# Kernel tuning notes

Measured on AMD Instinct MI355X. Metric: run time of the kernel, lower is better.

Reference implementation:

```python
import jax, jax.numpy as jnp
import numpy as np

B, T, I, H, F = 128, 256, 1024, 1024, 64


def setup_inputs() -> dict:
    key = jax.random.key(0)
    ks = jax.random.split(key, 12)
    s_ih = 1.0 / np.sqrt(I)
    s_hh = 1.0 / np.sqrt(H)
    s_fp = 1.0 / np.sqrt(F)
    def mk(k, shape, s):
        return jax.random.uniform(k, shape, jnp.float32, -s, s)
    inp = {
        "seq_input": jax.random.normal(ks[0], (B, T, I), jnp.float32),
        "field_pos": jax.random.normal(ks[1], (B, T, F), jnp.float32),
        # forward-direction cell params
        "W_ih_f": mk(ks[2], (4 * H, I), s_ih),
        "W_hh_f": mk(ks[3], (4 * H, H), s_hh),
        "b_f": mk(ks[4], (4 * H,), s_hh),
        "W_fp_f": mk(ks[5], (2 * H, F), s_fp),
        "b_fp_f": mk(ks[6], (2 * H,), s_fp),
        # backward-direction cell params
        "W_ih_b": mk(ks[7], (4 * H, I), s_ih),
        "W_hh_b": mk(ks[8], (4 * H, H), s_hh),
        "b_b": mk(ks[9], (4 * H,), s_hh),
        "W_fp_b": mk(ks[10], (2 * H, F), s_fp),
        "b_fp_b": mk(ks[11], (2 * H,), s_fp),
    }
    return inp


def _run_direction(xs, fps, W_ih, W_hh, b, W_fp, b_fp, rev):
    # xs: [T, B, I], fps: [T, B, F]  (time-major for scan)
    batch = xs.shape[1]
    h0 = jnp.zeros((batch, H), xs.dtype)
    c0 = jnp.zeros((batch, H), xs.dtype)

    def step(carry, inp):
        h, c = carry
        x, fp = inp
        gates = x @ W_ih.T + h @ W_hh.T + b            # [B, 4H]
        i_g, f_g, g_g, o_g = jnp.split(gates, 4, axis=-1)
        i_g = jax.nn.sigmoid(i_g)
        f_g = jax.nn.sigmoid(f_g)
        g_g = jnp.tanh(g_g)
        o_g = jax.nn.sigmoid(o_g)
        fg = fp @ W_fp.T + b_fp                        # [B, 2H] field gate
        l_g = jax.nn.sigmoid(fg[:, :H])
        d_g = jnp.tanh(fg[:, H:])
        c = f_g * c + i_g * g_g + l_g * d_g
        h = o_g * jnp.tanh(c)
        return (h, c), h

    (h_n, c_n), outs = jax.lax.scan(step, (h0, c0), (xs, fps), reverse=rev)
    # outs: [T, B, H] in original time order (scan with reverse=True already
    # restores forward ordering of stacked outputs, matching reverse(outputs))
    return outs, h_n, c_n


def reference(seq_input, field_pos,
              W_ih_f, W_hh_f, b_f, W_fp_f, b_fp_f,
              W_ih_b, W_hh_b, b_b, W_fp_b, b_fp_b):
    xs = jnp.swapaxes(seq_input, 0, 1)   # [T, B, I]
    fps = jnp.swapaxes(field_pos, 0, 1)  # [T, B, F]
    out_f, hf, cf = _run_direction(xs, fps, W_ih_f, W_hh_f, b_f, W_fp_f, b_fp_f, False)
    out_b, hb, cb = _run_direction(xs, fps, W_ih_b, W_hh_b, b_b, W_fp_b, b_fp_b, True)
    outputs = jnp.concatenate([out_f, out_b], axis=-1)   # [T, B, 2H] (torch.stack is seq-major)
    h_n = jnp.stack([hf, hb], axis=0)                    # [2, B, H]
    c_n = jnp.stack([cf, cb], axis=0)
    return outputs, h_n, c_n
```

## Files before the change

### kernel.cpp

```cpp
#include <hip/hip_runtime.h>
#include <hip/hip_bf16.h>


#define Bn 128
#define Tn 256
#define In 1024
#define Hn 1024
#define Fn 64

typedef __attribute__((ext_vector_type(8))) short short8;
typedef __attribute__((ext_vector_type(4))) short short4v;
typedef __attribute__((ext_vector_type(4))) float f32x4;

__device__ __forceinline__ unsigned short f2bf(float f) {
  __hip_bfloat16 h = __float2bfloat16(f);
  return *reinterpret_cast<unsigned short*>(&h);
}
__device__ __forceinline__ float sigm(float x) { return 1.0f / (1.0f + __expf(-x)); }
__device__ __forceinline__ float tanh_(float x) { return 1.0f - 2.0f / (1.0f + __expf(2.0f * x)); }

__global__ void f32_to_bf16_vec(const float* __restrict__ src, short* __restrict__ dst, int n4) {
  for (int i = blockIdx.x * blockDim.x + threadIdx.x; i < n4; i += gridDim.x * blockDim.x) {
    const float4 v = ((const float4*)src)[i];
    short4v o;
    o[0] = (short)f2bf(v.x); o[1] = (short)f2bf(v.y);
    o[2] = (short)f2bf(v.z); o[3] = (short)f2bf(v.w);
    ((short4v*)dst)[i] = o;
  }
}

__global__ void init_state(float* __restrict__ c_state, unsigned int* __restrict__ h0w) {
  const int i = blockIdx.x * blockDim.x + threadIdx.x;
  if (i < 2 * Bn * Hn) c_state[i] = 0.0f;
  if (i < (2 * Bn * Hn) / 2) h0w[i] = 0u;
}

__global__ __launch_bounds__(256) void lstm_step(
    const short* __restrict__ seq, const short* __restrict__ fpos,
    const short* __restrict__ Wih_f, const short* __restrict__ Whh_f,
    const short* __restrict__ Wfp_f,
    const short* __restrict__ Wih_b, const short* __restrict__ Whh_b,
    const short* __restrict__ Wfp_b,
    const float* __restrict__ b_f,  const float* __restrict__ bfp_f,
    const float* __restrict__ b_b,  const float* __restrict__ bfp_b,
    float* __restrict__ c_state,
    const short* __restrict__ h_read, short* __restrict__ h_write,
    float* __restrict__ out, int s)
{
  const int utile = blockIdx.x;
  const int mtile = blockIdx.y;
  const int dir   = blockIdx.z;
  const int t = dir ? (Tn - 1 - s) : s;
  const int j0 = utile * 16, m0 = mtile * 64;
  const int tid = threadIdx.x;
  const int lane = tid & 63, w = tid >> 6;
  const int l15 = lane & 15, lk = lane >> 4;

  const short* Wih = dir ? Wih_b : Wih_f;
  const short* Whh = dir ? Whh_b : Whh_f;
  const short* Wfp = dir ? Wfp_b : Wfp_f;
  const float* bg  = dir ? b_b   : b_f;
  const float* bfp = dir ? bfp_b : bfp_f;

  const int abat = m0 + 16 * w + l15;
  const short* xrow = seq    + ((size_t)abat * Tn + t) * In + lk * 8;
  const short* hrow = h_read + ((size_t)dir * Bn + abat) * Hn + lk * 8;

  f32x4 acc[4];
#pragma unroll
  for (int nf = 0; nf < 4; ++nf) acc[nf] = (f32x4){0.f, 0.f, 0.f, 0.f};

  const short* wr_ih[4];
  const short* wr_hh[4];
#pragma unroll
  for (int nf = 0; nf < 4; ++nf) {
    const int row = nf * Hn + j0 + l15;
    wr_ih[nf] = Wih + (size_t)row * In + lk * 8;
    wr_hh[nf] = Whh + (size_t)row * Hn + lk * 8;
  }

  for (int k = 0; k < In; k += 32) {
    const short8 a = *(const short8*)(xrow + k);
#pragma unroll
    for (int nf = 0; nf < 4; ++nf) {
      const short8 b = *(const short8*)(wr_ih[nf] + k);
      acc[nf] = __builtin_amdgcn_mfma_f32_16x16x32_bf16(a, b, acc[nf], 0, 0, 0);
    }
  }
  for (int k = 0; k < Hn; k += 32) {
    const short8 a = *(const short8*)(hrow + k);
#pragma unroll
    for (int nf = 0; nf < 4; ++nf) {
      const short8 b = *(const short8*)(wr_hh[nf] + k);
      acc[nf] = __builtin_amdgcn_mfma_f32_16x16x32_bf16(a, b, acc[nf], 0, 0, 0);
    }
  }

  f32x4 accf[2];
#pragma unroll
  for (int nf = 0; nf < 2; ++nf) accf[nf] = (f32x4){0.f, 0.f, 0.f, 0.f};
  const short* frow = fpos + ((size_t)abat * Tn + t) * Fn + lk * 8;
#pragma unroll
  for (int k = 0; k < Fn; k += 32) {
    const short8 a = *(const short8*)(frow + k);
#pragma unroll
    for (int nf = 0; nf < 2; ++nf) {
      const short8 b = *(const short8*)(Wfp + (size_t)(nf * Hn + j0 + l15) * Fn + lk * 8 + k);
      accf[nf] = __builtin_amdgcn_mfma_f32_16x16x32_bf16(a, b, accf[nf], 0, 0, 0);
    }
  }

  __shared__ float lds[4][64][17];
  __shared__ float ldsf[2][64][17];
#pragma unroll
  for (int nf = 0; nf < 4; ++nf)
#pragma unroll
    for (int r = 0; r < 4; ++r)
      lds[nf][16 * w + lk * 4 + r][l15] = acc[nf][r];
#pragma unroll
  for (int nf = 0; nf < 2; ++nf)
#pragma unroll
    for (int r = 0; r < 4; ++r)
      ldsf[nf][16 * w + lk * 4 + r][l15] = accf[nf][r];
  __syncthreads();

  const size_t OUTN = (size_t)Tn * Bn * 2 * Hn;
#pragma unroll
  for (int q = 0; q < 4; ++q) {
    const int p = tid + 256 * q;
    const int ml = p >> 4, jl = p & 15;
    const int bat = m0 + ml, j = j0 + jl;
    const float i_g = sigm (lds[0][ml][jl] + bg[j]);
    const float f_g = sigm (lds[1][ml][jl] + bg[Hn + j]);
    const float g_g = tanh_(lds[2][ml][jl] + bg[2 * Hn + j]);
    const float o_g = sigm (lds[3][ml][jl] + bg[3 * Hn + j]);
    const float l_g = sigm (ldsf[0][ml][jl] + bfp[j]);
    const float d_g = tanh_(ldsf[1][ml][jl] + bfp[Hn + j]);
    const size_t cidx = ((size_t)dir * Bn + bat) * Hn + j;
    const float c_new = f_g * c_state[cidx] + i_g * g_g + l_g * d_g;
    const float h_new = o_g * tanh_(c_new);
    c_state[cidx] = c_new;
    h_write[cidx] = (short)f2bf(h_new);
    out[((size_t)t * Bn + bat) * (2 * Hn) + (size_t)dir * Hn + j] = h_new;
    if (s == Tn - 1) {
      out[OUTN + cidx] = h_new;
      out[OUTN + (size_t)2 * Bn * Hn + cidx] = c_new;
    }
  }
}

static inline void conv(const void* src, short* dst, size_t n, hipStream_t stream) {
  int n4 = (int)(n / 4);
  int blocks = (n4 + 255) / 256; if (blocks > 8192) blocks = 8192;
  hipLaunchKernelGGL(f32_to_bf16_vec, dim3(blocks), dim3(256), 0, stream,
                     (const float*)src, dst, n4);
}

extern "C" void kernel_launch(void* const* d_in, const int* in_sizes, int n_in,
                              void* d_out, int out_size, void* d_ws, size_t ws_size,
                              hipStream_t stream) {
  (void)in_sizes; (void)n_in; (void)out_size; (void)ws_size;
  const float* b_f   = (const float*)d_in[4];
  const float* bfp_f = (const float*)d_in[6];
  const float* b_b   = (const float*)d_in[9];
  const float* bfp_b = (const float*)d_in[11];

  char* p = (char*)d_ws;
  float* c_state = (float*)p;            p += (size_t)2 * Bn * Hn * 4;
  short* h0      = (short*)p;            p += (size_t)2 * Bn * Hn * 2;
  short* h1      = (short*)p;            p += (size_t)2 * Bn * Hn * 2;
  short* seq_bf  = (short*)p;            p += (size_t)Bn * Tn * In * 2;
  short* fpos_bf = (short*)p;            p += (size_t)Bn * Tn * Fn * 2;
  short* Wih_bf[2], *Whh_bf[2], *Wfp_bf[2];
  for (int d = 0; d < 2; ++d) { Wih_bf[d] = (short*)p; p += (size_t)4 * Hn * In * 2; }
  for (int d = 0; d < 2; ++d) { Whh_bf[d] = (short*)p; p += (size_t)4 * Hn * Hn * 2; }
  for (int d = 0; d < 2; ++d) { Wfp_bf[d] = (short*)p; p += (size_t)2 * Hn * Fn * 2; }
  float* out = (float*)d_out;

  conv(d_in[0], seq_bf,   (size_t)Bn * Tn * In, stream);
  conv(d_in[1], fpos_bf,  (size_t)Bn * Tn * Fn, stream);
  conv(d_in[2], Wih_bf[0], (size_t)4 * Hn * In, stream);
  conv(d_in[3], Whh_bf[0], (size_t)4 * Hn * Hn, stream);
  conv(d_in[5], Wfp_bf[0], (size_t)2 * Hn * Fn, stream);
  conv(d_in[7], Wih_bf[1], (size_t)4 * Hn * In, stream);
  conv(d_in[8], Whh_bf[1], (size_t)4 * Hn * Hn, stream);
  conv(d_in[10], Wfp_bf[1], (size_t)2 * Hn * Fn, stream);

  hipLaunchKernelGGL(init_state, dim3((2 * Bn * Hn + 255) / 256), dim3(256), 0, stream,
                     c_state, (unsigned int*)h0);

  for (int s = 0; s < Tn; ++s) {
    const short* hr = (s & 1) ? h1 : h0;
    short* hw       = (s & 1) ? h0 : h1;
    hipLaunchKernelGGL(lstm_step, dim3(64, 2, 2), dim3(256), 0, stream,
                       seq_bf, fpos_bf,
                       Wih_bf[0], Whh_bf[0], Wfp_bf[0],
                       Wih_bf[1], Whh_bf[1], Wfp_bf[1],
                       b_f, bfp_f, b_b, bfp_b,
                       c_state, hr, hw, out, s);
  }
}
```

Baseline: 10.60 ms.

## Hoist input and field-gate projections out of the recurrence into chunked batched GEMMs

The input-to-hidden and field-position projections no longer run inside each per-timestep kernel. They are now computed for chunks of 32 timesteps by large batched GEMM kernels that write bf16 gate pre-activations, bias included. The per-step kernel then only does the recurrent h@W_hh^T product, with 512 threads per block, and adds the precomputed gates. This removes the serial dependence of the x-projection and lets it run at full GEMM parallelism, at the cost of extra workspace and bf16 rounding of the precomputed gates.

```diff
diff --git a/kernel.cpp b/kernel.cpp
--- a/kernel.cpp
+++ b/kernel.cpp
@@ -7,11 +7,17 @@
 #define In 1024
 #define Hn 1024
 #define Fn 64
+#define CH 32
 
 typedef __attribute__((ext_vector_type(8))) short short8;
 typedef __attribute__((ext_vector_type(4))) short short4v;
 typedef __attribute__((ext_vector_type(4))) float f32x4;
 
+__device__ __forceinline__ float bf2f(short u) {
+  union { unsigned int i; float f; } x;
+  x.i = ((unsigned int)(unsigned short)u) << 16;
+  return x.f;
+}
 __device__ __forceinline__ unsigned short f2bf(float f) {
   __hip_bfloat16 h = __float2bfloat16(f);
   return *reinterpret_cast<unsigned short*>(&h);
@@ -35,107 +41,159 @@
   if (i < (2 * Bn * Hn) / 2) h0w[i] = 0u;
 }
 
-__global__ __launch_bounds__(256) void lstm_step(
-    const short* __restrict__ seq, const short* __restrict__ fpos,
-    const short* __restrict__ Wih_f, const short* __restrict__ Whh_f,
-    const short* __restrict__ Wfp_f,
-    const short* __restrict__ Wih_b, const short* __restrict__ Whh_b,
-    const short* __restrict__ Wfp_b,
-    const float* __restrict__ b_f,  const float* __restrict__ bfp_f,
-    const float* __restrict__ b_b,  const float* __restrict__ bfp_b,
+__global__ __launch_bounds__(512) void precompute_gx(
+    const short* __restrict__ seq_bf,
+    const short* __restrict__ Wih_f, const short* __restrict__ Wih_b,
+    const float* __restrict__ b_f, const float* __restrict__ b_b,
+    short* __restrict__ gx, int c0)
+{
+  const int n0 = blockIdx.x * 64;
+  const int row0 = blockIdx.y * 64;
+  const int dir = blockIdx.z;
+  const int tid = threadIdx.x, lane = tid & 63, w = tid >> 6;
+  const int l15 = lane & 15, lk = lane >> 4;
+  const int mf = w & 3, nfp = w >> 2;
+
+  const short* Wih = dir ? Wih_b : Wih_f;
+  const float* bg  = dir ? b_b   : b_f;
+
+  const int grow = row0 + mf * 16 + l15;
+  const int sl = grow >> 7, bat = grow & 127;
+  const int t = dir ? (Tn - 1 - (c0 + sl)) : (c0 + sl);
+  const short* xrow = seq_bf + ((size_t)bat * Tn + t) * In + lk * 8;
+
+  const short* br[2];
+#pragma unroll
+  for (int q = 0; q < 2; ++q)
+    br[q] = Wih + (size_t)(n0 + (nfp * 2 + q) * 16 + l15) * In + lk * 8;
+
+  f32x4 acc[2];
+  acc[0] = (f32x4){0.f,0.f,0.f,0.f}; acc[1] = (f32x4){0.f,0.f,0.f,0.f};
+  for (int k = 0; k < In; k += 32) {
+    const short8 a = *(const short8*)(xrow + k);
+#pragma unroll
+    for (int q = 0; q < 2; ++q) {
+      const short8 b = *(const short8*)(br[q] + k);
+      acc[q] = __builtin_amdgcn_mfma_f32_16x16x32_bf16(a, b, acc[q], 0, 0, 0);
+    }
+  }
+#pragma unroll
+  for (int q = 0; q < 2; ++q) {
+    const int col = n0 + (nfp * 2 + q) * 16 + l15;
+    const float bias = bg[col];
+#pragma unroll
+    for (int r = 0; r < 4; ++r) {
+      const int grow2 = row0 + mf * 16 + lk * 4 + r;
+      const int sl2 = grow2 >> 7, bat2 = grow2 & 127;
+      gx[(((size_t)dir * CH + sl2) * Bn + bat2) * (4 * Hn) + col] =
+          (short)f2bf(acc[q][r] + bias);
+    }
+  }
+}
+
+__global__ __launch_bounds__(512) void precompute_fg(
+    const short* __restrict__ fpos_bf,
+    const short* __restrict__ Wfp_f, const short* __restrict__ Wfp_b,
+    const float* __restrict__ bfp_f, const float* __restrict__ bfp_b,
+    short* __restrict__ fg, int c0)
+{
+  const int n0 = blockIdx.x * 64;
+  const int row0 = blockIdx.y * 64;
+  const int dir = blockIdx.z;
+  const int tid = threadIdx.x, lane = tid & 63, w = tid >> 6;
+  const int l15 = lane & 15, lk = lane >> 4;
+  const int mf = w & 3, nfp = w >> 2;
+
+  const short* Wfp = dir ? Wfp_b : Wfp_f;
+  const float* bfp = dir ? bfp_b : bfp_f;
+
+  const int grow = row0 + mf * 16 + l15;
+  const int sl = grow >> 7, bat = grow & 127;
+  const int t = dir ? (Tn - 1 - (c0 + sl)) : (c0 + sl);
+  const short* frow = fpos_bf + ((size_t)bat * Tn + t) * Fn + lk * 8;
+
+  f32x4 acc[2];
+  acc[0] = (f32x4){0.f,0.f,0.f,0.f}; acc[1] = (f32x4){0.f,0.f,0.f,0.f};
+#pragma unroll
+  for (int k = 0; k < Fn; k += 32) {
+    const short8 a = *(const short8*)(frow + k);
+#pragma unroll
+    for (int q = 0; q < 2; ++q) {
+      const short8 b = *(const short8*)(Wfp + (size_t)(n0 + (nfp * 2 + q) * 16 + l15) * Fn + lk * 8 + k);
+      acc[q] = __builtin_amdgcn_mfma_f32_16x16x32_bf16(a, b, acc[q], 0, 0, 0);
+    }
+  }
+#pragma unroll
+  for (int q = 0; q < 2; ++q) {
+    const int col = n0 + (nfp * 2 + q) * 16 + l15;
+    const float bias = bfp[col];
+#pragma unroll
+    for (int r = 0; r < 4; ++r) {
+      const int grow2 = row0 + mf * 16 + lk * 4 + r;
+      const int sl2 = grow2 >> 7, bat2 = grow2 & 127;
+      fg[(((size_t)dir * CH + sl2) * Bn + bat2) * (2 * Hn) + col] =
+          (short)f2bf(acc[q][r] + bias);
+    }
+  }
+}
+
+__global__ __launch_bounds__(512) void lstm_step2(
+    const short* __restrict__ Whh_f, const short* __restrict__ Whh_b,
+    const short* __restrict__ gx, const short* __restrict__ fg,
     float* __restrict__ c_state,
     const short* __restrict__ h_read, short* __restrict__ h_write,
-    float* __restrict__ out, int s)
+    float* __restrict__ out, int s, int sl)
 {
-  const int utile = blockIdx.x;
-  const int mtile = blockIdx.y;
-  const int dir   = blockIdx.z;
+  const int j0 = blockIdx.x * 16;
+  const int dir = blockIdx.y;
+  const int m0 = blockIdx.z * 64;
   const int t = dir ? (Tn - 1 - s) : s;
-  const int j0 = utile * 16, m0 = mtile * 64;
-  const int tid = threadIdx.x;
-  const int lane = tid & 63, w = tid >> 6;
+  const int tid = threadIdx.x, lane = tid & 63, w = tid >> 6;
   const int l15 = lane & 15, lk = lane >> 4;
-
-  const short* Wih = dir ? Wih_b : Wih_f;
+  const int mf = w & 3, nfp = w >> 2;
+
   const short* Whh = dir ? Whh_b : Whh_f;
-  const short* Wfp = dir ? Wfp_b : Wfp_f;
-  const float* bg  = dir ? b_b   : b_f;
-  const float* bfp = dir ? bfp_b : bfp_f;
-
-  const int abat = m0 + 16 * w + l15;
-  const short* xrow = seq    + ((size_t)abat * Tn + t) * In + lk * 8;
+
+  const int abat = m0 + mf * 16 + l15;
   const short* hrow = h_read + ((size_t)dir * Bn + abat) * Hn + lk * 8;
-
-  f32x4 acc[4];
-#pragma unroll
-  for (int nf = 0; nf < 4; ++nf) acc[nf] = (f32x4){0.f, 0.f, 0.f, 0.f};
-
-  const short* wr_ih[4];
-  const short* wr_hh[4];
-#pragma unroll
-  for (int nf = 0; nf < 4; ++nf) {
-    const int row = nf * Hn + j0 + l15;
-    wr_ih[nf] = Wih + (size_t)row * In + lk * 8;
-    wr_hh[nf] = Whh + (size_t)row * Hn + lk * 8;
-  }
-
-  for (int k = 0; k < In; k += 32) {
-    const short8 a = *(const short8*)(xrow + k);
-#pragma unroll
-    for (int nf = 0; nf < 4; ++nf) {
-      const short8 b = *(const short8*)(wr_ih[nf] + k);
-      acc[nf] = __builtin_amdgcn_mfma_f32_16x16x32_bf16(a, b, acc[nf], 0, 0, 0);
-    }
-  }
+  const short* br[2];
+#pragma unroll
+  for (int q = 0; q < 2; ++q)
+    br[q] = Whh + (size_t)((nfp * 2 + q) * Hn + j0 + l15) * Hn + lk * 8;
+
+  f32x4 acc[2];
+  acc[0] = (f32x4){0.f,0.f,0.f,0.f}; acc[1] = (f32x4){0.f,0.f,0.f,0.f};
   for (int k = 0; k < Hn; k += 32) {
     const short8 a = *(const short8*)(hrow + k);
 #pragma unroll
-    for (int nf = 0; nf < 4; ++nf) {
-      const short8 b = *(const short8*)(wr_hh[nf] + k);
-      acc[nf] = __builtin_amdgcn_mfma_f32_16x16x32_bf16(a, b, acc[nf], 0, 0, 0);
-    }
-  }
-
-  f32x4 accf[2];
-#pragma unroll
-  for (int nf = 0; nf < 2; ++nf) accf[nf] = (f32x4){0.f, 0.f, 0.f, 0.f};
-  const short* frow = fpos + ((size_t)abat * Tn + t) * Fn + lk * 8;
-#pragma unroll
-  for (int k = 0; k < Fn; k += 32) {
-    const short8 a = *(const short8*)(frow + k);
-#pragma unroll
-    for (int nf = 0; nf < 2; ++nf) {
-      const short8 b = *(const short8*)(Wfp + (size_t)(nf * Hn + j0 + l15) * Fn + lk * 8 + k);
-      accf[nf] = __builtin_amdgcn_mfma_f32_16x16x32_bf16(a, b, accf[nf], 0, 0, 0);
+    for (int q = 0; q < 2; ++q) {
+      const short8 b = *(const short8*)(br[q] + k);
+      acc[q] = __builtin_amdgcn_mfma_f32_16x16x32_bf16(a, b, acc[q], 0, 0, 0);
     }
   }
 
   __shared__ float lds[4][64][17];
-  __shared__ float ldsf[2][64][17];
-#pragma unroll
-  for (int nf = 0; nf < 4; ++nf)
+#pragma unroll
+  for (int q = 0; q < 2; ++q)
 #pragma unroll
     for (int r = 0; r < 4; ++r)
-      lds[nf][16 * w + lk * 4 + r][l15] = acc[nf][r];
-#pragma unroll
-  for (int nf = 0; nf < 2; ++nf)
-#pragma unroll
-    for (int r = 0; r < 4; ++r)
-      ldsf[nf][16 * w + lk * 4 + r][l15] = accf[nf][r];
+      lds[nfp * 2 + q][mf * 16 + lk * 4 + r][l15] = acc[q][r];
   __syncthreads();
 
   const size_t OUTN = (size_t)Tn * Bn * 2 * Hn;
 #pragma unroll
-  for (int q = 0; q < 4; ++q) {
-    const int p = tid + 256 * q;
+  for (int qq = 0; qq < 2; ++qq) {
+    const int p = tid + 512 * qq;
     const int ml = p >> 4, jl = p & 15;
     const int bat = m0 + ml, j = j0 + jl;
-    const float i_g = sigm (lds[0][ml][jl] + bg[j]);
-    const float f_g = sigm (lds[1][ml][jl] + bg[Hn + j]);
-    const float g_g = tanh_(lds[2][ml][jl] + bg[2 * Hn + j]);
-    const float o_g = sigm (lds[3][ml][jl] + bg[3 * Hn + j]);
-    const float l_g = sigm (ldsf[0][ml][jl] + bfp[j]);
-    const float d_g = tanh_(ldsf[1][ml][jl] + bfp[Hn + j]);
+    const short* gxb = gx + (((size_t)dir * CH + sl) * Bn + bat) * (4 * Hn);
+    const short* fgb = fg + (((size_t)dir * CH + sl) * Bn + bat) * (2 * Hn);
+    const float i_g = sigm (lds[0][ml][jl] + bf2f(gxb[j]));
+    const float f_g = sigm (lds[1][ml][jl] + bf2f(gxb[Hn + j]));
+    const float g_g = tanh_(lds[2][ml][jl] + bf2f(gxb[2 * Hn + j]));
+    const float o_g = sigm (lds[3][ml][jl] + bf2f(gxb[3 * Hn + j]));
+    const float l_g = sigm (bf2f(fgb[j]));
+    const float d_g = tanh_(bf2f(fgb[Hn + j]));
     const size_t cidx = ((size_t)dir * Bn + bat) * Hn + j;
     const float c_new = f_g * c_state[cidx] + i_g * g_g + l_g * d_g;
     const float h_new = o_g * tanh_(c_new);
@@ -175,10 +233,12 @@
   for (int d = 0; d < 2; ++d) { Wih_bf[d] = (short*)p; p += (size_t)4 * Hn * In * 2; }
   for (int d = 0; d < 2; ++d) { Whh_bf[d] = (short*)p; p += (size_t)4 * Hn * Hn * 2; }
   for (int d = 0; d < 2; ++d) { Wfp_bf[d] = (short*)p; p += (size_t)2 * Hn * Fn * 2; }
+  short* gx = (short*)p;                 p += (size_t)2 * CH * Bn * 4 * Hn * 2;
+  short* fgb = (short*)p;                p += (size_t)2 * CH * Bn * 2 * Hn * 2;
   float* out = (float*)d_out;
 
-  conv(d_in[0], seq_bf,   (size_t)Bn * Tn * In, stream);
-  conv(d_in[1], fpos_bf,  (size_t)Bn * Tn * Fn, stream);
+  conv(d_in[0], seq_bf,    (size_t)Bn * Tn * In, stream);
+  conv(d_in[1], fpos_bf,   (size_t)Bn * Tn * Fn, stream);
   conv(d_in[2], Wih_bf[0], (size_t)4 * Hn * In, stream);
   conv(d_in[3], Whh_bf[0], (size_t)4 * Hn * Hn, stream);
   conv(d_in[5], Wfp_bf[0], (size_t)2 * Hn * Fn, stream);
@@ -189,14 +249,18 @@
   hipLaunchKernelGGL(init_state, dim3((2 * Bn * Hn + 255) / 256), dim3(256), 0, stream,
                      c_state, (unsigned int*)h0);
 
-  for (int s = 0; s < Tn; ++s) {
-    const short* hr = (s & 1) ? h1 : h0;
-    short* hw       = (s & 1) ? h0 : h1;
-    hipLaunchKernelGGL(lstm_step, dim3(64, 2, 2), dim3(256), 0, stream,
-                       seq_bf, fpos_bf,
-                       Wih_bf[0], Whh_bf[0], Wfp_bf[0],
-                       Wih_bf[1], Whh_bf[1], Wfp_bf[1],
-                       b_f, bfp_f, b_b, bfp_b,
-                       c_state, hr, hw, out, s);
-  }
-}
+  for (int c = 0; c < Tn / CH; ++c) {
+    hipLaunchKernelGGL(precompute_gx, dim3(64, CH * Bn / 64, 2), dim3(512), 0, stream,
+                       seq_bf, Wih_bf[0], Wih_bf[1], b_f, b_b, gx, c * CH);
+    hipLaunchKernelGGL(precompute_fg, dim3(32, CH * Bn / 64, 2), dim3(512), 0, stream,
+                       fpos_bf, Wfp_bf[0], Wfp_bf[1], bfp_f, bfp_b, fgb, c * CH);
+    for (int sl = 0; sl < CH; ++sl) {
+      const int s = c * CH + sl;
+      const short* hr = (s & 1) ? h1 : h0;
+      short* hw       = (s & 1) ? h0 : h1;
+      hipLaunchKernelGGL(lstm_step2, dim3(64, 2, 2), dim3(512), 0, stream,
+                         Whh_bf[0], Whh_bf[1], gx, fgb,
+                         c_state, hr, hw, out, s, sl);
+    }
+  }
+}
```

Measured after the change: 12.56 ms. 1.19x slower.

## Replace per-step launches with persistent cooperative LSTM kernel and grid barrier

Applied to the files above, without the earlier changes.

The 256 per-timestep launches become a single cooperative kernel of 256 blocks, each owning 8 hidden units of one direction for the whole batch. The block's slice of W_hh stays in LDS, the cell state stays in registers, and a global atomic counter barrier separates timesteps. This removes launch overhead and repeated reloading of W_hh and c_state from global memory. The cost is a grid-wide spin barrier every step and dependence on all 256 blocks being co-resident.

```diff
diff --git a/kernel.cpp b/kernel.cpp
--- a/kernel.cpp
+++ b/kernel.cpp
@@ -7,6 +7,9 @@
 #define In 1024
 #define Hn 1024
 #define Fn 64
+#define NBLK 256
+#define UPB 8
+#define CNT_STRIDE 16
 
 typedef __attribute__((ext_vector_type(8))) short short8;
 typedef __attribute__((ext_vector_type(4))) short short4v;
@@ -29,122 +32,139 @@
   }
 }
 
-__global__ void init_state(float* __restrict__ c_state, unsigned int* __restrict__ h0w) {
+__global__ void init_state(int* __restrict__ cnts, unsigned int* __restrict__ h0w) {
   const int i = blockIdx.x * blockDim.x + threadIdx.x;
-  if (i < 2 * Bn * Hn) c_state[i] = 0.0f;
+  if (i < Tn * CNT_STRIDE) cnts[i] = 0;
   if (i < (2 * Bn * Hn) / 2) h0w[i] = 0u;
 }
 
-__global__ __launch_bounds__(256) void lstm_step(
-    const short* __restrict__ seq, const short* __restrict__ fpos,
+__global__ __launch_bounds__(512) void lstm_persist(
+    const short* __restrict__ seq_bf, const short* __restrict__ fpos_bf,
     const short* __restrict__ Wih_f, const short* __restrict__ Whh_f,
     const short* __restrict__ Wfp_f,
     const short* __restrict__ Wih_b, const short* __restrict__ Whh_b,
     const short* __restrict__ Wfp_b,
     const float* __restrict__ b_f,  const float* __restrict__ bfp_f,
     const float* __restrict__ b_b,  const float* __restrict__ bfp_b,
-    float* __restrict__ c_state,
-    const short* __restrict__ h_read, short* __restrict__ h_write,
-    float* __restrict__ out, int s)
+    short* __restrict__ h_buf,
+    int* __restrict__ cnts,
+    float* __restrict__ out)
 {
-  const int utile = blockIdx.x;
-  const int mtile = blockIdx.y;
-  const int dir   = blockIdx.z;
-  const int t = dir ? (Tn - 1 - s) : s;
-  const int j0 = utile * 16, m0 = mtile * 64;
+  const int bx = blockIdx.x;
+  const int dir = bx >> 7;
+  const int utile = bx & 127;
+  const int j0 = utile * UPB;
   const int tid = threadIdx.x;
   const int lane = tid & 63, w = tid >> 6;
   const int l15 = lane & 15, lk = lane >> 4;
 
-  const short* Wih = dir ? Wih_b : Wih_f;
-  const short* Whh = dir ? Whh_b : Whh_f;
-  const short* Wfp = dir ? Wfp_b : Wfp_f;
-  const float* bg  = dir ? b_b   : b_f;
-  const float* bfp = dir ? bfp_b : bfp_f;
-
-  const int abat = m0 + 16 * w + l15;
-  const short* xrow = seq    + ((size_t)abat * Tn + t) * In + lk * 8;
-  const short* hrow = h_read + ((size_t)dir * Bn + abat) * Hn + lk * 8;
-
-  f32x4 acc[4];
-#pragma unroll
-  for (int nf = 0; nf < 4; ++nf) acc[nf] = (f32x4){0.f, 0.f, 0.f, 0.f};
-
-  const short* wr_ih[4];
-  const short* wr_hh[4];
-#pragma unroll
-  for (int nf = 0; nf < 4; ++nf) {
-    const int row = nf * Hn + j0 + l15;
-    wr_ih[nf] = Wih + (size_t)row * In + lk * 8;
-    wr_hh[nf] = Whh + (size_t)row * Hn + lk * 8;
-  }
-
-  for (int k = 0; k < In; k += 32) {
-    const short8 a = *(const short8*)(xrow + k);
-#pragma unroll
-    for (int nf = 0; nf < 4; ++nf) {
-      const short8 b = *(const short8*)(wr_ih[nf] + k);
-      acc[nf] = __builtin_amdgcn_mfma_f32_16x16x32_bf16(a, b, acc[nf], 0, 0, 0);
-    }
-  }
-  for (int k = 0; k < Hn; k += 32) {
-    const short8 a = *(const short8*)(hrow + k);
-#pragma unroll
-    for (int nf = 0; nf < 4; ++nf) {
-      const short8 b = *(const short8*)(wr_hh[nf] + k);
-      acc[nf] = __builtin_amdgcn_mfma_f32_16x16x32_bf16(a, b, acc[nf], 0, 0, 0);
-    }
-  }
-
-  f32x4 accf[2];
-#pragma unroll
-  for (int nf = 0; nf < 2; ++nf) accf[nf] = (f32x4){0.f, 0.f, 0.f, 0.f};
-  const short* frow = fpos + ((size_t)abat * Tn + t) * Fn + lk * 8;
-#pragma unroll
-  for (int k = 0; k < Fn; k += 32) {
-    const short8 a = *(const short8*)(frow + k);
-#pragma unroll
-    for (int nf = 0; nf < 2; ++nf) {
-      const short8 b = *(const short8*)(Wfp + (size_t)(nf * Hn + j0 + l15) * Fn + lk * 8 + k);
-      accf[nf] = __builtin_amdgcn_mfma_f32_16x16x32_bf16(a, b, accf[nf], 0, 0, 0);
-    }
-  }
-
-  __shared__ float lds[4][64][17];
-  __shared__ float ldsf[2][64][17];
-#pragma unroll
-  for (int nf = 0; nf < 4; ++nf)
-#pragma unroll
-    for (int r = 0; r < 4; ++r)
-      lds[nf][16 * w + lk * 4 + r][l15] = acc[nf][r];
-#pragma unroll
-  for (int nf = 0; nf < 2; ++nf)
-#pragma unroll
-    for (int r = 0; r < 4; ++r)
-      ldsf[nf][16 * w + lk * 4 + r][l15] = accf[nf][r];
+  const short* Wih_g = dir ? Wih_b : Wih_f;
+  const short* Whh_g = dir ? Whh_b : Whh_f;
+  const short* Wfp_g = dir ? Wfp_b : Wfp_f;
+  const float* bg    = dir ? b_b   : b_f;
+  const float* bfpg  = dir ? bfp_b : bfp_f;
+
+  __shared__ short whh_s[32][1032];
+  __shared__ float xch[128][33];
+  __shared__ float fxch[128][17];
+
+  {
+    const int row = tid >> 4;
+    const int cb = (tid & 15) * 64;
+    const int grow = (row >> 3) * Hn + j0 + (row & 7);
+#pragma unroll
+    for (int i = 0; i < 8; ++i)
+      *(short8*)&whh_s[row][cb + i * 8] =
+          *(const short8*)(Whh_g + (size_t)grow * In + cb + i * 8);
+  }
+  short8 bq[2];
+  {
+    const int frow = (l15 < 8) ? (j0 + l15) : (Hn + j0 + (l15 - 8));
+#pragma unroll
+    for (int it = 0; it < 2; ++it)
+      bq[it] = *(const short8*)(Wfp_g + (size_t)frow * Fn + it * 32 + lk * 8);
+  }
+  const int u = tid & 7;
+  const int jj = j0 + u;
+  const float bi = bg[jj], bff = bg[Hn + jj], bgg = bg[2 * Hn + jj], bo = bg[3 * Hn + jj];
+  const float bl = bfpg[jj], bd = bfpg[Hn + jj];
+  float creg[2] = {0.f, 0.f};
+
+  const int abat = w * 16 + l15;
+  const int c0 = l15, c1 = 16 + l15;
+  const short* wxp0 = Wih_g + (size_t)((c0 >> 3) * Hn + j0 + (c0 & 7)) * In + lk * 8;
+  const short* wxp1 = Wih_g + (size_t)((c1 >> 3) * Hn + j0 + (c1 & 7)) * In + lk * 8;
+  const short* hb0 = &whh_s[c0][lk * 8];
+  const short* hb1 = &whh_s[c1][lk * 8];
+
   __syncthreads();
 
   const size_t OUTN = (size_t)Tn * Bn * 2 * Hn;
-#pragma unroll
-  for (int q = 0; q < 4; ++q) {
-    const int p = tid + 256 * q;
-    const int ml = p >> 4, jl = p & 15;
-    const int bat = m0 + ml, j = j0 + jl;
-    const float i_g = sigm (lds[0][ml][jl] + bg[j]);
-    const float f_g = sigm (lds[1][ml][jl] + bg[Hn + j]);
-    const float g_g = tanh_(lds[2][ml][jl] + bg[2 * Hn + j]);
-    const float o_g = sigm (lds[3][ml][jl] + bg[3 * Hn + j]);
-    const float l_g = sigm (ldsf[0][ml][jl] + bfp[j]);
-    const float d_g = tanh_(ldsf[1][ml][jl] + bfp[Hn + j]);
-    const size_t cidx = ((size_t)dir * Bn + bat) * Hn + j;
-    const float c_new = f_g * c_state[cidx] + i_g * g_g + l_g * d_g;
-    const float h_new = o_g * tanh_(c_new);
-    c_state[cidx] = c_new;
-    h_write[cidx] = (short)f2bf(h_new);
-    out[((size_t)t * Bn + bat) * (2 * Hn) + (size_t)dir * Hn + j] = h_new;
-    if (s == Tn - 1) {
-      out[OUTN + cidx] = h_new;
-      out[OUTN + (size_t)2 * Bn * Hn + cidx] = c_new;
+
+  for (int s = 0; s < Tn; ++s) {
+    const int t = dir ? (Tn - 1 - s) : s;
+    const int pr = s & 1, pw = pr ^ 1;
+
+    f32x4 acc0 = (f32x4){0.f, 0.f, 0.f, 0.f};
+    f32x4 acc1 = (f32x4){0.f, 0.f, 0.f, 0.f};
+
+    const short* xrow = seq_bf + ((size_t)abat * Tn + t) * In + lk * 8;
+    for (int k = 0; k < In; k += 32) {
+      const short8 a = *(const short8*)(xrow + k);
+      acc0 = __builtin_amdgcn_mfma_f32_16x16x32_bf16(a, *(const short8*)(wxp0 + k), acc0, 0, 0, 0);
+      acc1 = __builtin_amdgcn_mfma_f32_16x16x32_bf16(a, *(const short8*)(wxp1 + k), acc1, 0, 0, 0);
+    }
+    const short* hrow = h_buf + (((size_t)pr * 2 + dir) * Bn + abat) * Hn + lk * 8;
+    for (int k = 0; k < Hn; k += 32) {
+      const short8 a = *(const short8*)(hrow + k);
+      acc0 = __builtin_amdgcn_mfma_f32_16x16x32_bf16(a, *(const short8*)(hb0 + k), acc0, 0, 0, 0);
+      acc1 = __builtin_amdgcn_mfma_f32_16x16x32_bf16(a, *(const short8*)(hb1 + k), acc1, 0, 0, 0);
+    }
+    f32x4 accf = (f32x4){0.f, 0.f, 0.f, 0.f};
+    const short* frow = fpos_bf + ((size_t)abat * Tn + t) * Fn + lk * 8;
+    accf = __builtin_amdgcn_mfma_f32_16x16x32_bf16(*(const short8*)frow, bq[0], accf, 0, 0, 0);
+    accf = __builtin_amdgcn_mfma_f32_16x16x32_bf16(*(const short8*)(frow + 32), bq[1], accf, 0, 0, 0);
+
+#pragma unroll
+    for (int r = 0; r < 4; ++r) {
+      const int brow = w * 16 + lk * 4 + r;
+      xch[brow][l15] = acc0[r];
+      xch[brow][16 + l15] = acc1[r];
+      fxch[brow][l15] = accf[r];
+    }
+    __syncthreads();
+
+#pragma unroll
+    for (int q2 = 0; q2 < 2; ++q2) {
+      const int bat = (tid >> 3) + q2 * 64;
+      const float i_g = sigm (xch[bat][u] + bi);
+      const float f_g = sigm (xch[bat][8 + u] + bff);
+      const float g_g = tanh_(xch[bat][16 + u] + bgg);
+      const float o_g = sigm (xch[bat][24 + u] + bo);
+      const float l_g = sigm (fxch[bat][u] + bl);
+      const float d_g = tanh_(fxch[bat][8 + u] + bd);
+      const float c_new = f_g * creg[q2] + i_g * g_g + l_g * d_g;
+      const float h_new = o_g * tanh_(c_new);
+      creg[q2] = c_new;
+      h_buf[(((size_t)pw * 2 + dir) * Bn + bat) * Hn + jj] = (short)f2bf(h_new);
+      out[((size_t)t * Bn + bat) * (2 * Hn) + (size_t)dir * Hn + jj] = h_new;
+      if (s == Tn - 1) {
+        out[OUTN + ((size_t)dir * Bn + bat) * Hn + jj] = h_new;
+        out[OUTN + (size_t)2 * Bn * Hn + ((size_t)dir * Bn + bat) * Hn + jj] = c_new;
+      }
+    }
+
+    if (s < Tn - 1) {
+      __syncthreads();
+      if (tid == 0) {
+        __threadfence();
+        atomicAdd(&cnts[s * CNT_STRIDE], 1);
+        while (__hip_atomic_load(&cnts[s * CNT_STRIDE], __ATOMIC_RELAXED,
+                                 __HIP_MEMORY_SCOPE_AGENT) < NBLK)
+          __builtin_amdgcn_s_sleep(1);
+      }
+      __syncthreads();
+      __threadfence();
     }
   }
 }
@@ -166,37 +186,35 @@
   const float* bfp_b = (const float*)d_in[11];
 
   char* p = (char*)d_ws;
-  float* c_state = (float*)p;            p += (size_t)2 * Bn * Hn * 4;
-  short* h0      = (short*)p;            p += (size_t)2 * Bn * Hn * 2;
-  short* h1      = (short*)p;            p += (size_t)2 * Bn * Hn * 2;
+  int*   cnts  = (int*)p;                p += (size_t)Tn * CNT_STRIDE * 4;
+  short* h_buf = (short*)p;              p += (size_t)2 * 2 * Bn * Hn * 2;
   short* seq_bf  = (short*)p;            p += (size_t)Bn * Tn * In * 2;
   short* fpos_bf = (short*)p;            p += (size_t)Bn * Tn * Fn * 2;
-  short* Wih_bf[2], *Whh_bf[2], *Wfp_bf[2];
+  short *Wih_bf[2], *Whh_bf[2], *Wfp_bf[2];
   for (int d = 0; d < 2; ++d) { Wih_bf[d] = (short*)p; p += (size_t)4 * Hn * In * 2; }
   for (int d = 0; d < 2; ++d) { Whh_bf[d] = (short*)p; p += (size_t)4 * Hn * Hn * 2; }
   for (int d = 0; d < 2; ++d) { Wfp_bf[d] = (short*)p; p += (size_t)2 * Hn * Fn * 2; }
   float* out = (float*)d_out;
 
-  conv(d_in[0], seq_bf,   (size_t)Bn * Tn * In, stream);
-  conv(d_in[1], fpos_bf,  (size_t)Bn * Tn * Fn, stream);
-  conv(d_in[2], Wih_bf[0], (size_t)4 * Hn * In, stream);
-  conv(d_in[3], Whh_bf[0], (size_t)4 * Hn * Hn, stream);
-  conv(d_in[5], Wfp_bf[0], (size_t)2 * Hn * Fn, stream);
-  conv(d_in[7], Wih_bf[1], (size_t)4 * Hn * In, stream);
-  conv(d_in[8], Whh_bf[1], (size_t)4 * Hn * Hn, stream);
+  conv(d_in[0],  seq_bf,    (size_t)Bn * Tn * In, stream);
+  conv(d_in[1],  fpos_bf,   (size_t)Bn * Tn * Fn, stream);
+  conv(d_in[2],  Wih_bf[0], (size_t)4 * Hn * In, stream);
+  conv(d_in[3],  Whh_bf[0], (size_t)4 * Hn * Hn, stream);
+  conv(d_in[5],  Wfp_bf[0], (size_t)2 * Hn * Fn, stream);
+  conv(d_in[7],  Wih_bf[1], (size_t)4 * Hn * In, stream);
+  conv(d_in[8],  Whh_bf[1], (size_t)4 * Hn * Hn, stream);
   conv(d_in[10], Wfp_bf[1], (size_t)2 * Hn * Fn, stream);
 
-  hipLaunchKernelGGL(init_state, dim3((2 * Bn * Hn + 255) / 256), dim3(256), 0, stream,
-                     c_state, (unsigned int*)h0);
-
-  for (int s = 0; s < Tn; ++s) {
-    const short* hr = (s & 1) ? h1 : h0;
-    short* hw       = (s & 1) ? h0 : h1;
-    hipLaunchKernelGGL(lstm_step, dim3(64, 2, 2), dim3(256), 0, stream,
-                       seq_bf, fpos_bf,
-                       Wih_bf[0], Whh_bf[0], Wfp_bf[0],
-                       Wih_bf[1], Whh_bf[1], Wfp_bf[1],
-                       b_f, bfp_f, b_b, bfp_b,
-                       c_state, hr, hw, out, s);
-  }
-}
+  hipLaunchKernelGGL(init_state, dim3(512), dim3(256), 0, stream,
+                     cnts, (unsigned int*)h_buf);
+
+  void* args[] = {
+    (void*)&seq_bf, (void*)&fpos_bf,
+    (void*)&Wih_bf[0], (void*)&Whh_bf[0], (void*)&Wfp_bf[0],
+    (void*)&Wih_bf[1], (void*)&Whh_bf[1], (void*)&Wfp_bf[1],
+    (void*)&b_f, (void*)&bfp_f, (void*)&b_b, (void*)&bfp_b,
+    (void*)&h_buf, (void*)&cnts, (void*)&out
+  };
+  hipLaunchCooperativeKernel((void*)lstm_persist, dim3(NBLK), dim3(512),
+                             args, 0, stream);
+}
```

Measured after the change: 18.81 ms. +77.5%, slower.
